# Optimization experiments

Measured on AMD Instinct MI355X. Metric: run time of the kernel, lower is better.

Reference implementation:

```python
import jax, jax.numpy as jnp
import numpy as np

N_BALL = 256
N_EDGES = N_BALL * (N_BALL - 1)  # fully connected, no self loops
BATCH = 4
F_IN = 64
H = 64  # out_channels
EDGE_TYPES = 2


def _edge_structure():
    # receiver repeated pattern / sender covering all other nodes, as in NRI
    recv, send = [], []
    for r in range(N_BALL):
        for s in range(N_BALL):
            if s != r:
                recv.append(r)
                send.append(s)
    eye = np.eye(N_BALL, dtype=np.float32)
    rel_rec = eye[np.array(recv)]   # [E, N]
    rel_send = eye[np.array(send)]  # [E, N]
    return jnp.asarray(rel_rec), jnp.asarray(rel_send)


def setup_inputs() -> dict:
    key = jax.random.key(0)
    ks = jax.random.split(key, 12)
    rel_rec, rel_send = _edge_structure()
    s1 = 1.0 / np.sqrt(2 * F_IN)
    s2 = 1.0 / np.sqrt(H)
    s3 = 1.0 / np.sqrt(F_IN + H)
    return {
        "inputs": jax.random.normal(ks[0], (BATCH, N_BALL, F_IN), jnp.float32),
        "rel_type": jax.random.uniform(ks[1], (BATCH, N_EDGES, EDGE_TYPES), jnp.float32),
        "rel_rec": rel_rec,
        "rel_send": rel_send,
        # per-edge-type message MLPs (stacked over edge types)
        "W1": jax.random.uniform(ks[2], (EDGE_TYPES, 2 * F_IN, H), jnp.float32, -s1, s1),
        "b1": jax.random.uniform(ks[3], (EDGE_TYPES, H), jnp.float32, -s1, s1),
        "W2": jax.random.uniform(ks[4], (EDGE_TYPES, H, H), jnp.float32, -s2, s2),
        "b2": jax.random.uniform(ks[5], (EDGE_TYPES, H), jnp.float32, -s2, s2),
        # output MLP
        "Wo1": jax.random.uniform(ks[6], (F_IN + H, H), jnp.float32, -s3, s3),
        "bo1": jax.random.uniform(ks[7], (H,), jnp.float32, -s3, s3),
        "Wo2": jax.random.uniform(ks[8], (H, H), jnp.float32, -s2, s2),
        "bo2": jax.random.uniform(ks[9], (H,), jnp.float32, -s2, s2),
    }


def reference(inputs, rel_type, rel_rec, rel_send, W1, b1, W2, b2, Wo1, bo1, Wo2, bo2):
    # gather node features onto edges via one-hot matmuls
    receivers = jnp.einsum('en,bnf->bef', rel_rec, inputs)   # [B,E,F]
    senders = jnp.einsum('en,bnf->bef', rel_send, inputs)    # [B,E,F]
    pre_msg = jnp.concatenate([senders, receivers], axis=-1)  # [B,E,2F]

    all_msgs = jnp.zeros(pre_msg.shape[:2] + (H,), dtype=pre_msg.dtype)
    for i in range(EDGE_TYPES):  # skip_first=False -> start at 0
        msg = jax.nn.relu(pre_msg @ W1[i] + b1[i])
        msg = jax.nn.relu(msg @ W2[i] + b2[i])
        all_msgs = all_msgs + msg * rel_type[:, :, i:i + 1]

    # scatter-aggregate edge messages back to receiver nodes
    agg_msgs = jnp.einsum('beh,en->bnh', all_msgs, rel_rec)   # [B,N,H]
    aug_inputs = jnp.concatenate([inputs, agg_msgs], axis=-1)  # [B,N,F+H]

    pred = jax.nn.relu(aug_inputs @ Wo1 + bo1)
    pred = jax.nn.relu(pred @ Wo2 + bo2)
    return inputs + pred
```

## Files before the change

### kernel.cpp

```cpp
#include <hip/hip_runtime.h>

#define BATCH 4
#define NB    256
#define NE    (NB*(NB-1))
#define FIN   64
#define HD    64

typedef short  short8  __attribute__((ext_vector_type(8)));
typedef float  f32x16  __attribute__((ext_vector_type(16)));

__device__ __forceinline__ short f2bf(float x) {
    unsigned u = __builtin_bit_cast(unsigned, x);
    u += 0x7fffu + ((u >> 16) & 1u);
    return (short)(u >> 16);
}

__global__ __launch_bounds__(64) void prep_kernel(
    const float* __restrict__ x,
    const float* __restrict__ W1,
    const float* __restrict__ b1,
    const float* __restrict__ W2,
    float* __restrict__ Psw,
    float* __restrict__ Q,
    short* __restrict__ W2f)
{
    const int blk = blockIdx.x;
    const int t   = threadIdx.x;
    __shared__ float xl[FIN];

    if (blk < 2 * BATCH * NB) {
        const int i   = blk >> 10;
        const int rem = blk & 1023;
        const int b   = rem >> 8;
        const int n   = rem & 255;
        xl[t] = x[(b * NB + n) * FIN + t];
        __syncthreads();
        const float* w1s = W1 + i * 128 * 64;
        const float* w1r = W1 + i * 128 * 64 + 64 * 64;
        float accP = 0.f;
        float accQ = b1[i * 64 + t];
        #pragma unroll 8
        for (int f = 0; f < 64; ++f) {
            float xv = xl[f];
            accP = fmaf(xv, w1s[f * 64 + t], accP);
            accQ = fmaf(xv, w1r[f * 64 + t], accQ);
        }
        Psw[(((i * BATCH + b) * 8 + (t >> 3)) * NB + n) * 8 + (t & 7)] = accP;
        Q[((i * BATCH + b) * NB + n) * 64 + t] = accQ;
    } else {
        #pragma unroll
        for (int i = 0; i < 2; ++i)
            #pragma unroll
            for (int nt = 0; nt < 2; ++nt)
                #pragma unroll
                for (int k0 = 0; k0 < 4; ++k0)
                    #pragma unroll
                    for (int j = 0; j < 8; ++j) {
                        int k = k0 * 16 + 8 * (t >> 5) + j;
                        int n = (t & 31) + 32 * nt;
                        W2f[(((i * 2 + nt) * 4 + k0) * 64 + t) * 8 + j] =
                            f2bf(W2[(i * 64 + k) * 64 + n]);
                    }
    }
}

__global__ __launch_bounds__(256) void main_kernel(
    const float* __restrict__ x,
    const float* __restrict__ rel_type,
    const float* __restrict__ b2,
    const float* __restrict__ Wo1,
    const float* __restrict__ bo1,
    const float* __restrict__ Wo2,
    const float* __restrict__ bo2,
    const float* __restrict__ Psw,
    const float* __restrict__ Q,
    const short* __restrict__ W2f,
    float* __restrict__ out)
{
    const int b = blockIdx.x >> 8;
    const int r = blockIdx.x & 255;
    const int t = threadIdx.x;
    const int lane = t & 63;
    const int w    = t >> 6;

    __shared__ __align__(16) float rt[256][2];
    __shared__ __align__(16) float qrow[2][64];
    __shared__ __align__(16) float b2l[2][64];
    __shared__ __align__(16) float red[4][64];
    __shared__ __align__(16) float aggl[64];
    __shared__ __align__(16) float xl[64];
    __shared__ __align__(16) float predl[64];

    if (t < 255) {
        const float* p = rel_type + ((size_t)b * NE + (size_t)r * 255 + t) * 2;
        rt[t][0] = p[0];
        rt[t][1] = p[1];
    } else if (t == 255) {
        rt[255][0] = 0.f; rt[255][1] = 0.f;
    }
    if (t < 128) {
        int i = t >> 6, h = t & 63;
        qrow[i][h] = Q[((i * BATCH + b) * NB + r) * 64 + h];
        b2l[i][h]  = b2[i * 64 + h];
    }
    if (t < 64) xl[t] = x[(b * NB + r) * FIN + t];
    __syncthreads();

    const int l31 = lane & 31;
    const int lh  = lane >> 5;

    const int k0m = 64 * w + l31;
    const int k1m = 64 * w + 32 + l31;
    int s0 = (k0m < r) ? k0m : k0m + 1; if (s0 > 255) s0 = 255;
    int s1 = (k1m < r) ? k1m : k1m + 1; if (s1 > 255) s1 = 255;

    float psum0 = 0.f, psum1 = 0.f;

    #pragma unroll
    for (int i = 0; i < 2; ++i) {
        const float* Pb = Psw + (size_t)(i * BATCH + b) * 8 * NB * 8;
        const short* wf = W2f + (size_t)i * 2 * 4 * 64 * 8;

        short8 Bf[2][4];
        #pragma unroll
        for (int nt = 0; nt < 2; ++nt)
            #pragma unroll
            for (int k0 = 0; k0 < 4; ++k0)
                Bf[nt][k0] = *(const short8*)(wf + ((nt * 4 + k0) * 64 + lane) * 8);

        f32x16 acc00 = {}, acc01 = {}, acc10 = {}, acc11 = {};

        #pragma unroll
        for (int k0 = 0; k0 < 4; ++k0) {
            const int hb = 2 * k0 + lh;
            const int h0 = hb * 8;
            float4 pa0 = *(const float4*)(Pb + (hb * NB + s0) * 8);
            float4 pa1 = *(const float4*)(Pb + (hb * NB + s0) * 8 + 4);
            float4 pb0 = *(const float4*)(Pb + (hb * NB + s1) * 8);
            float4 pb1 = *(const float4*)(Pb + (hb * NB + s1) * 8 + 4);
            float4 q0  = *(const float4*)(&qrow[i][h0]);
            float4 q1  = *(const float4*)(&qrow[i][h0 + 4]);

            short8 a0, a1;
            a0[0] = f2bf(fmaxf(pa0.x + q0.x, 0.f));
            a0[1] = f2bf(fmaxf(pa0.y + q0.y, 0.f));
            a0[2] = f2bf(fmaxf(pa0.z + q0.z, 0.f));
            a0[3] = f2bf(fmaxf(pa0.w + q0.w, 0.f));
            a0[4] = f2bf(fmaxf(pa1.x + q1.x, 0.f));
            a0[5] = f2bf(fmaxf(pa1.y + q1.y, 0.f));
            a0[6] = f2bf(fmaxf(pa1.z + q1.z, 0.f));
            a0[7] = f2bf(fmaxf(pa1.w + q1.w, 0.f));
            a1[0] = f2bf(fmaxf(pb0.x + q0.x, 0.f));
            a1[1] = f2bf(fmaxf(pb0.y + q0.y, 0.f));
            a1[2] = f2bf(fmaxf(pb0.z + q0.z, 0.f));
            a1[3] = f2bf(fmaxf(pb0.w + q0.w, 0.f));
            a1[4] = f2bf(fmaxf(pb1.x + q1.x, 0.f));
            a1[5] = f2bf(fmaxf(pb1.y + q1.y, 0.f));
            a1[6] = f2bf(fmaxf(pb1.z + q1.z, 0.f));
            a1[7] = f2bf(fmaxf(pb1.w + q1.w, 0.f));

            acc00 = __builtin_amdgcn_mfma_f32_32x32x16_bf16(a0, Bf[0][k0], acc00, 0, 0, 0);
            acc01 = __builtin_amdgcn_mfma_f32_32x32x16_bf16(a0, Bf[1][k0], acc01, 0, 0, 0);
            acc10 = __builtin_amdgcn_mfma_f32_32x32x16_bf16(a1, Bf[0][k0], acc10, 0, 0, 0);
            acc11 = __builtin_amdgcn_mfma_f32_32x32x16_bf16(a1, Bf[1][k0], acc11, 0, 0, 0);
        }

        const float b2v0 = b2l[i][l31];
        const float b2v1 = b2l[i][l31 + 32];
        #pragma unroll
        for (int reg = 0; reg < 16; ++reg) {
            const int rowoff = (reg & 3) + 8 * (reg >> 2) + 4 * lh;
            const float rt0 = rt[64 * w + rowoff][i];
            const float rt1 = rt[64 * w + 32 + rowoff][i];
            psum0 += fmaxf(acc00[reg] + b2v0, 0.f) * rt0;
            psum1 += fmaxf(acc01[reg] + b2v1, 0.f) * rt0;
            psum0 += fmaxf(acc10[reg] + b2v0, 0.f) * rt1;
            psum1 += fmaxf(acc11[reg] + b2v1, 0.f) * rt1;
        }
    }

    psum0 += __shfl_xor(psum0, 32, 64);
    psum1 += __shfl_xor(psum1, 32, 64);
    if ((lane & 32) == 0) {
        red[w][l31]      = psum0;
        red[w][l31 + 32] = psum1;
    }
    __syncthreads();
    if (t < 64) aggl[t] = red[0][t] + red[1][t] + red[2][t] + red[3][t];
    __syncthreads();

    {
        const int h = t & 63, part = t >> 6;
        const int j0 = part * 32;
        float s = 0.f;
        #pragma unroll 8
        for (int jj = 0; jj < 32; ++jj) {
            const int j = j0 + jj;
            const float a = (j < 64) ? xl[j] : aggl[j - 64];
            s = fmaf(a, Wo1[j * 64 + h], s);
        }
        red[part][h] = s;
    }
    __syncthreads();
    if (t < 64) {
        float s = red[0][t] + red[1][t] + red[2][t] + red[3][t] + bo1[t];
        predl[t] = fmaxf(s, 0.f);
    }
    __syncthreads();

    {
        const int h = t & 63, part = t >> 6;
        const int j0 = part * 16;
        float s = 0.f;
        #pragma unroll 8
        for (int jj = 0; jj < 16; ++jj) {
            const int j = j0 + jj;
            s = fmaf(predl[j], Wo2[j * 64 + h], s);
        }
        red[part][h] = s;
    }
    __syncthreads();
    if (t < 64) {
        float s = red[0][t] + red[1][t] + red[2][t] + red[3][t] + bo2[t];
        out[((size_t)b * NB + r) * 64 + t] = xl[t] + fmaxf(s, 0.f);
    }
}

extern "C" void kernel_launch(void* const* d_in, const int* in_sizes, int n_in,
                              void* d_out, int out_size, void* d_ws, size_t ws_size,
                              hipStream_t stream) {
    (void)in_sizes; (void)n_in; (void)out_size; (void)ws_size;

    const float* x    = (const float*)d_in[0];
    const float* rt   = (const float*)d_in[1];
    const float* W1   = (const float*)d_in[4];
    const float* b1   = (const float*)d_in[5];
    const float* W2   = (const float*)d_in[6];
    const float* b2   = (const float*)d_in[7];
    const float* Wo1  = (const float*)d_in[8];
    const float* bo1  = (const float*)d_in[9];
    const float* Wo2  = (const float*)d_in[10];
    const float* bo2  = (const float*)d_in[11];
    float* out = (float*)d_out;

    char* ws = (char*)d_ws;
    float* Psw = (float*)ws;
    float* Q   = (float*)(ws + 524288);
    short* W2f = (short*)(ws + 1048576);

    prep_kernel<<<2 * BATCH * NB + 1, 64, 0, stream>>>(x, W1, b1, W2, Psw, Q, W2f);
    main_kernel<<<BATCH * NB, 256, 0, stream>>>(x, rt, b2, Wo1, bo1, Wo2, bo2,
                                                Psw, Q, W2f, out);
}
```

Measured before the change: 25.80 us.

## Store sender projections as bf16, stage W2 in LDS, pre-transpose output MLP weights

The precomputed sender projection P is now stored as bf16, which halves the per-edge gather traffic in the main kernel. The prep kernel now processes 4 nodes per 256-thread block and adds blocks that pre-transpose Wo1 and Wo2, so the output MLP reads contiguous float4 weight vectors prefetched into registers before the reduction. W2 fragments are copied into LDS per block instead of being loaded into registers from global memory. Rounding P to bf16 before adding Q adds an extra rounding step, and the 16 KB LDS buffer may reduce occupancy.

```diff
diff --git a/kernel.cpp b/kernel.cpp
--- a/kernel.cpp
+++ b/kernel.cpp
@@ -1,66 +1,82 @@
 #include <hip/hip_runtime.h>
+#include <hip/hip_bf16.h>
 
 #define BATCH 4
 #define NB    256
 #define NE    (NB*(NB-1))
-#define FIN   64
-#define HD    64
 
 typedef short  short8  __attribute__((ext_vector_type(8)));
 typedef float  f32x16  __attribute__((ext_vector_type(16)));
 
 __device__ __forceinline__ short f2bf(float x) {
-    unsigned u = __builtin_bit_cast(unsigned, x);
-    u += 0x7fffu + ((u >> 16) & 1u);
-    return (short)(u >> 16);
-}
-
-__global__ __launch_bounds__(64) void prep_kernel(
+    __hip_bfloat16 h = __float2bfloat16(x);
+    return __builtin_bit_cast(short, h);
+}
+__device__ __forceinline__ float bf2f(short s) {
+    unsigned u = ((unsigned)(unsigned short)s) << 16;
+    return __builtin_bit_cast(float, u);
+}
+
+__global__ __launch_bounds__(256) void prep_kernel(
     const float* __restrict__ x,
     const float* __restrict__ W1,
     const float* __restrict__ b1,
     const float* __restrict__ W2,
-    float* __restrict__ Psw,
+    const float* __restrict__ Wo1,
+    const float* __restrict__ Wo2,
+    short* __restrict__ Pbf,
     float* __restrict__ Q,
-    short* __restrict__ W2f)
+    short* __restrict__ W2f,
+    float* __restrict__ Wo1T,
+    float* __restrict__ Wo2T)
 {
+    __shared__ float xl[4][64];
     const int blk = blockIdx.x;
     const int t   = threadIdx.x;
-    __shared__ float xl[FIN];
-
-    if (blk < 2 * BATCH * NB) {
-        const int i   = blk >> 10;
-        const int rem = blk & 1023;
-        const int b   = rem >> 8;
-        const int n   = rem & 255;
-        xl[t] = x[(b * NB + n) * FIN + t];
+
+    if (blk < 512) {
+        const int i   = blk >> 8;
+        const int rem = blk & 255;
+        const int b   = rem >> 6;
+        const int g   = t >> 6;
+        const int n   = (rem & 63) * 4 + g;
+        const int h   = t & 63;
+        xl[g][h] = x[(b * NB + n) * 64 + h];
         __syncthreads();
-        const float* w1s = W1 + i * 128 * 64;
-        const float* w1r = W1 + i * 128 * 64 + 64 * 64;
+        const float* w1s = W1 + i * 8192;
+        const float* w1r = w1s + 4096;
         float accP = 0.f;
-        float accQ = b1[i * 64 + t];
-        #pragma unroll 8
+        float accQ = b1[i * 64 + h];
+        #pragma unroll 16
         for (int f = 0; f < 64; ++f) {
-            float xv = xl[f];
-            accP = fmaf(xv, w1s[f * 64 + t], accP);
-            accQ = fmaf(xv, w1r[f * 64 + t], accQ);
-        }
-        Psw[(((i * BATCH + b) * 8 + (t >> 3)) * NB + n) * 8 + (t & 7)] = accP;
-        Q[((i * BATCH + b) * NB + n) * 64 + t] = accQ;
+            const float xv = xl[g][f];
+            accP = fmaf(xv, w1s[f * 64 + h], accP);
+            accQ = fmaf(xv, w1r[f * 64 + h], accQ);
+        }
+        Pbf[(((i * BATCH + b) * 8 + (h >> 3)) * NB + n) * 8 + (h & 7)] = f2bf(accP);
+        Q[((i * BATCH + b) * NB + n) * 64 + h] = accQ;
+    } else if (blk == 512) {
+        #pragma unroll
+        for (int q = 0; q < 32; ++q) {
+            const int e  = q * 256 + t;
+            const int j  = e & 7, ln = (e >> 3) & 63, k0 = (e >> 9) & 3,
+                      nt = (e >> 11) & 1, i = e >> 12;
+            const int k  = k0 * 16 + 8 * (ln >> 5) + j;
+            const int n  = (ln & 31) + 32 * nt;
+            W2f[e] = f2bf(W2[(i * 64 + k) * 64 + n]);
+        }
+    } else if (blk == 513) {
+        #pragma unroll
+        for (int q = 0; q < 32; ++q) {
+            const int e = q * 256 + t;
+            Wo1T[e] = Wo1[(e & 127) * 64 + (e >> 7)];
+        }
     } else {
         #pragma unroll
-        for (int i = 0; i < 2; ++i)
-            #pragma unroll
-            for (int nt = 0; nt < 2; ++nt)
-                #pragma unroll
-                for (int k0 = 0; k0 < 4; ++k0)
-                    #pragma unroll
-                    for (int j = 0; j < 8; ++j) {
-                        int k = k0 * 16 + 8 * (t >> 5) + j;
-                        int n = (t & 31) + 32 * nt;
-                        W2f[(((i * 2 + nt) * 4 + k0) * 64 + t) * 8 + j] =
-                            f2bf(W2[(i * 64 + k) * 64 + n]);
-                    }
+        for (int q = 0; q < 16; ++q) {
+            const int e = q * 256 + t;
+            Wo2T[e] = Wo2[(e & 63) * 64 + (e >> 6)];
+        }
     }
 }
 
@@ -68,13 +84,13 @@
     const float* __restrict__ x,
     const float* __restrict__ rel_type,
     const float* __restrict__ b2,
-    const float* __restrict__ Wo1,
     const float* __restrict__ bo1,
-    const float* __restrict__ Wo2,
     const float* __restrict__ bo2,
-    const float* __restrict__ Psw,
+    const short* __restrict__ Pbf,
     const float* __restrict__ Q,
     const short* __restrict__ W2f,
+    const float* __restrict__ Wo1T,
+    const float* __restrict__ Wo2T,
     float* __restrict__ out)
 {
     const int b = blockIdx.x >> 8;
@@ -82,35 +98,40 @@
     const int t = threadIdx.x;
     const int lane = t & 63;
     const int w    = t >> 6;
+    const int l31  = lane & 31;
+    const int lh   = lane >> 5;
 
     __shared__ __align__(16) float rt[256][2];
     __shared__ __align__(16) float qrow[2][64];
     __shared__ __align__(16) float b2l[2][64];
+    __shared__ __align__(16) short W2l[8192];
     __shared__ __align__(16) float red[4][64];
+    __shared__ __align__(16) float xl[64];
     __shared__ __align__(16) float aggl[64];
-    __shared__ __align__(16) float xl[64];
     __shared__ __align__(16) float predl[64];
 
     if (t < 255) {
         const float* p = rel_type + ((size_t)b * NE + (size_t)r * 255 + t) * 2;
         rt[t][0] = p[0];
         rt[t][1] = p[1];
-    } else if (t == 255) {
+    } else {
         rt[255][0] = 0.f; rt[255][1] = 0.f;
     }
+    #pragma unroll
+    for (int q = 0; q < 4; ++q) {
+        const int e = (q * 256 + t) * 8;
+        *(short8*)(W2l + e) = *(const short8*)(W2f + e);
+    }
     if (t < 128) {
-        int i = t >> 6, h = t & 63;
+        const int i = t >> 6, h = t & 63;
         qrow[i][h] = Q[((i * BATCH + b) * NB + r) * 64 + h];
         b2l[i][h]  = b2[i * 64 + h];
     }
-    if (t < 64) xl[t] = x[(b * NB + r) * FIN + t];
-    __syncthreads();
-
-    const int l31 = lane & 31;
-    const int lh  = lane >> 5;
+    if (t >= 128 && t < 192) xl[t - 128] = x[(b * NB + r) * 64 + (t - 128)];
+    __syncthreads();
 
     const int k0m = 64 * w + l31;
-    const int k1m = 64 * w + 32 + l31;
+    const int k1m = k0m + 32;
     int s0 = (k0m < r) ? k0m : k0m + 1; if (s0 > 255) s0 = 255;
     int s1 = (k1m < r) ? k1m : k1m + 1; if (s1 > 255) s1 = 255;
 
@@ -118,51 +139,33 @@
 
     #pragma unroll
     for (int i = 0; i < 2; ++i) {
-        const float* Pb = Psw + (size_t)(i * BATCH + b) * 8 * NB * 8;
-        const short* wf = W2f + (size_t)i * 2 * 4 * 64 * 8;
-
-        short8 Bf[2][4];
-        #pragma unroll
-        for (int nt = 0; nt < 2; ++nt)
-            #pragma unroll
-            for (int k0 = 0; k0 < 4; ++k0)
-                Bf[nt][k0] = *(const short8*)(wf + ((nt * 4 + k0) * 64 + lane) * 8);
-
-        f32x16 acc00 = {}, acc01 = {}, acc10 = {}, acc11 = {};
-
+        const short* Pb = Pbf + (size_t)(i * BATCH + b) * (8 * NB * 8);
+
+        short8 L0[4], L1[4];
         #pragma unroll
         for (int k0 = 0; k0 < 4; ++k0) {
             const int hb = 2 * k0 + lh;
-            const int h0 = hb * 8;
-            float4 pa0 = *(const float4*)(Pb + (hb * NB + s0) * 8);
-            float4 pa1 = *(const float4*)(Pb + (hb * NB + s0) * 8 + 4);
-            float4 pb0 = *(const float4*)(Pb + (hb * NB + s1) * 8);
-            float4 pb1 = *(const float4*)(Pb + (hb * NB + s1) * 8 + 4);
-            float4 q0  = *(const float4*)(&qrow[i][h0]);
-            float4 q1  = *(const float4*)(&qrow[i][h0 + 4]);
-
+            L0[k0] = *(const short8*)(Pb + (hb * NB + s0) * 8);
+            L1[k0] = *(const short8*)(Pb + (hb * NB + s1) * 8);
+        }
+
+        f32x16 acc00 = {}, acc01 = {}, acc10 = {}, acc11 = {};
+        #pragma unroll
+        for (int k0 = 0; k0 < 4; ++k0) {
+            const int h0 = (2 * k0 + lh) * 8;
             short8 a0, a1;
-            a0[0] = f2bf(fmaxf(pa0.x + q0.x, 0.f));
-            a0[1] = f2bf(fmaxf(pa0.y + q0.y, 0.f));
-            a0[2] = f2bf(fmaxf(pa0.z + q0.z, 0.f));
-            a0[3] = f2bf(fmaxf(pa0.w + q0.w, 0.f));
-            a0[4] = f2bf(fmaxf(pa1.x + q1.x, 0.f));
-            a0[5] = f2bf(fmaxf(pa1.y + q1.y, 0.f));
-            a0[6] = f2bf(fmaxf(pa1.z + q1.z, 0.f));
-            a0[7] = f2bf(fmaxf(pa1.w + q1.w, 0.f));
-            a1[0] = f2bf(fmaxf(pb0.x + q0.x, 0.f));
-            a1[1] = f2bf(fmaxf(pb0.y + q0.y, 0.f));
-            a1[2] = f2bf(fmaxf(pb0.z + q0.z, 0.f));
-            a1[3] = f2bf(fmaxf(pb0.w + q0.w, 0.f));
-            a1[4] = f2bf(fmaxf(pb1.x + q1.x, 0.f));
-            a1[5] = f2bf(fmaxf(pb1.y + q1.y, 0.f));
-            a1[6] = f2bf(fmaxf(pb1.z + q1.z, 0.f));
-            a1[7] = f2bf(fmaxf(pb1.w + q1.w, 0.f));
-
-            acc00 = __builtin_amdgcn_mfma_f32_32x32x16_bf16(a0, Bf[0][k0], acc00, 0, 0, 0);
-            acc01 = __builtin_amdgcn_mfma_f32_32x32x16_bf16(a0, Bf[1][k0], acc01, 0, 0, 0);
-            acc10 = __builtin_amdgcn_mfma_f32_32x32x16_bf16(a1, Bf[0][k0], acc10, 0, 0, 0);
-            acc11 = __builtin_amdgcn_mfma_f32_32x32x16_bf16(a1, Bf[1][k0], acc11, 0, 0, 0);
+            #pragma unroll
+            for (int e = 0; e < 8; ++e) {
+                const float qv = qrow[i][h0 + e];
+                a0[e] = f2bf(fmaxf(bf2f(L0[k0][e]) + qv, 0.f));
+                a1[e] = f2bf(fmaxf(bf2f(L1[k0][e]) + qv, 0.f));
+            }
+            const short8 B0 = *(const short8*)(W2l + ((i * 8 + k0) * 64 + lane) * 8);
+            const short8 B1 = *(const short8*)(W2l + ((i * 8 + 4 + k0) * 64 + lane) * 8);
+            acc00 = __builtin_amdgcn_mfma_f32_32x32x16_bf16(a0, B0, acc00, 0, 0, 0);
+            acc01 = __builtin_amdgcn_mfma_f32_32x32x16_bf16(a0, B1, acc01, 0, 0, 0);
+            acc10 = __builtin_amdgcn_mfma_f32_32x32x16_bf16(a1, B0, acc10, 0, 0, 0);
+            acc11 = __builtin_amdgcn_mfma_f32_32x32x16_bf16(a1, B1, acc11, 0, 0, 0);
         }
 
         const float b2v0 = b2l[i][l31];
@@ -179,9 +182,18 @@
         }
     }
 
+    float4 wv1[8];
+    #pragma unroll
+    for (int q = 0; q < 8; ++q)
+        wv1[q] = *(const float4*)(Wo1T + lane * 128 + w * 32 + q * 4);
+    float4 wv2[4];
+    #pragma unroll
+    for (int q = 0; q < 4; ++q)
+        wv2[q] = *(const float4*)(Wo2T + lane * 64 + w * 16 + q * 4);
+
     psum0 += __shfl_xor(psum0, 32, 64);
     psum1 += __shfl_xor(psum1, 32, 64);
-    if ((lane & 32) == 0) {
+    if (lh == 0) {
         red[w][l31]      = psum0;
         red[w][l31 + 32] = psum1;
     }
@@ -190,40 +202,33 @@
     __syncthreads();
 
     {
-        const int h = t & 63, part = t >> 6;
-        const int j0 = part * 32;
+        const float* src = (w < 2) ? (xl + w * 32) : (aggl + (w - 2) * 32);
         float s = 0.f;
-        #pragma unroll 8
-        for (int jj = 0; jj < 32; ++jj) {
-            const int j = j0 + jj;
-            const float a = (j < 64) ? xl[j] : aggl[j - 64];
-            s = fmaf(a, Wo1[j * 64 + h], s);
-        }
-        red[part][h] = s;
-    }
-    __syncthreads();
-    if (t < 64) {
-        float s = red[0][t] + red[1][t] + red[2][t] + red[3][t] + bo1[t];
-        predl[t] = fmaxf(s, 0.f);
-    }
+        #pragma unroll
+        for (int q = 0; q < 8; ++q)
+            #pragma unroll
+            for (int e = 0; e < 4; ++e)
+                s = fmaf(src[q * 4 + e], wv1[q][e], s);
+        red[w][lane] = s;
+    }
+    __syncthreads();
+    if (t < 64)
+        predl[t] = fmaxf(red[0][t] + red[1][t] + red[2][t] + red[3][t] + bo1[t], 0.f);
     __syncthreads();
 
     {
-        const int h = t & 63, part = t >> 6;
-        const int j0 = part * 16;
         float s = 0.f;
-        #pragma unroll 8
-        for (int jj = 0; jj < 16; ++jj) {
-            const int j = j0 + jj;
-            s = fmaf(predl[j], Wo2[j * 64 + h], s);
-        }
-        red[part][h] = s;
-    }
-    __syncthreads();
-    if (t < 64) {
-        float s = red[0][t] + red[1][t] + red[2][t] + red[3][t] + bo2[t];
-        out[((size_t)b * NB + r) * 64 + t] = xl[t] + fmaxf(s, 0.f);
-    }
+        #pragma unroll
+        for (int q = 0; q < 4; ++q)
+            #pragma unroll
+            for (int e = 0; e < 4; ++e)
+                s = fmaf(predl[w * 16 + q * 4 + e], wv2[q][e], s);
+        red[w][lane] = s;
+    }
+    __syncthreads();
+    if (t < 64)
+        out[((size_t)b * NB + r) * 64 + t] =
+            xl[t] + fmaxf(red[0][t] + red[1][t] + red[2][t] + red[3][t] + bo2[t], 0.f);
 }
 
 extern "C" void kernel_launch(void* const* d_in, const int* in_sizes, int n_in,
@@ -244,11 +249,14 @@
     float* out = (float*)d_out;
 
     char* ws = (char*)d_ws;
-    float* Psw = (float*)ws;
-    float* Q   = (float*)(ws + 524288);
-    short* W2f = (short*)(ws + 1048576);
-
-    prep_kernel<<<2 * BATCH * NB + 1, 64, 0, stream>>>(x, W1, b1, W2, Psw, Q, W2f);
-    main_kernel<<<BATCH * NB, 256, 0, stream>>>(x, rt, b2, Wo1, bo1, Wo2, bo2,
-                                                Psw, Q, W2f, out);
-}
+    short* Pbf  = (short*)ws;
+    float* Q    = (float*)(ws + 262144);
+    short* W2f  = (short*)(ws + 786432);
+    float* Wo1T = (float*)(ws + 802816);
+    float* Wo2T = (float*)(ws + 835584);
+
+    prep_kernel<<<515, 256, 0, stream>>>(x, W1, b1, W2, Wo1, Wo2,
+                                         Pbf, Q, W2f, Wo1T, Wo2T);
+    main_kernel<<<BATCH * NB, 256, 0, stream>>>(x, rt, b2, bo1, bo2,
+                                                Pbf, Q, W2f, Wo1T, Wo2T, out);
+}
```

Result: slower. 26.98 us (+4.6%).
